# Performance work log

Measured on AMD Instinct MI355X. Metric: run time of the kernel, lower is better.

## Reference

```python
import jax, jax.numpy as jnp
import numpy as np

N = 100000   # nodes
E = 3200000  # edges (avg degree 32)
G = 1024     # graphs in batch
H = 16       # hidden_dim


def setup_inputs() -> dict:
    key = jax.random.key(0)
    ks = jax.random.split(key, 12)
    p = lambda k, s: jax.random.normal(k, s, dtype=jnp.float32) * 0.1
    return {
        "types": jax.random.randint(ks[0], (N,), 0, 3),
        "pos": jax.random.randint(ks[1], (N,), 0, 3),
        "edge_index": jax.random.randint(ks[2], (2, E), 0, N),
        "batch": jnp.sort(jax.random.randint(ks[3], (N,), 0, G)),
        "W1": p(ks[4], (3, H)), "b1": jnp.zeros((H,), jnp.float32),
        "W2": p(ks[5], (3, H)), "b2": jnp.zeros((H,), jnp.float32),
        "Wg0": p(ks[6], (2 * H, H)), "bg0": jnp.zeros((H,), jnp.float32),
        "Wg1": p(ks[7], (H, H)), "bg1": jnp.zeros((H,), jnp.float32),
        "Wg2": p(ks[8], (H, H)), "bg2": jnp.zeros((H,), jnp.float32),
        "Wo": p(ks[9], (H, 1)), "bo": jnp.zeros((1,), jnp.float32),
    }


def reference(types, pos, edge_index, batch, W1, b1, W2, b2,
              Wg0, bg0, Wg1, bg1, Wg2, bg2, Wo, bo):
    # one-hot encode + linear embed
    xt = jax.nn.one_hot(types, 3, dtype=jnp.float32) @ W1 + b1   # [N, H]
    xp = jax.nn.one_hot(pos, 3, dtype=jnp.float32) @ W2 + b2     # [N, H]
    z = jnp.concatenate([xt, xp], axis=-1)                        # [N, 2H]

    src, dst = edge_index[0], edge_index[1]
    # GCN symmetric normalization with self-loops (gcn_norm)
    deg = jax.ops.segment_sum(jnp.ones((E,), jnp.float32), dst, num_segments=N) + 1.0
    dis = jax.lax.rsqrt(deg)                                      # D^{-1/2}
    edge_coef = (dis[src] * dis[dst])[:, None]                    # [E, 1]
    self_coef = (dis * dis)[:, None]                              # [N, 1]

    def gcn_conv(x, W, b):
        h = x @ W                                                 # [N, H]
        agg = jax.ops.segment_sum(h[src] * edge_coef, dst, num_segments=N)
        return agg + h * self_coef + b

    z = jax.nn.relu(gcn_conv(z, Wg0, bg0))  # dropout=0.2 is train-only; eval mode
    z = jax.nn.relu(gcn_conv(z, Wg1, bg1))
    z = gcn_conv(z, Wg2, bg2)               # no act after last layer

    # global_mean_pool over graph ids
    cnt = jax.ops.segment_sum(jnp.ones((N,), jnp.float32), batch, num_segments=G)
    pooled = jax.ops.segment_sum(z, batch, num_segments=G) / jnp.maximum(cnt, 1.0)[:, None]
    return pooled @ Wo + bo                                       # [G, 1]
```

## Files before the change

### kernel.cpp

```cpp
#include <hip/hip_runtime.h>
#include <hip/hip_fp16.h>

#define NN 100000
#define NE 3200000
#define NG 1024
#define NP 100352
#define NBUCK 391
#define NBLK 256
#define CHUNK ((NE + NBLK - 1) / NBLK)
#define WINCAP 12288

static __device__ inline void acc_u2(float4& acc, uint2 u) {
    __half2* ph = reinterpret_cast<__half2*>(&u);
    float2 lo = __half22float2(ph[0]);
    float2 hi = __half22float2(ph[1]);
    acc.x += lo.x; acc.y += lo.y; acc.z += hi.x; acc.w += hi.y;
}
static __device__ inline uint2 pack4(float a, float b, float c, float d) {
    __half2 lo = __floats2half2_rn(a, b);
    __half2 hi = __floats2half2_rn(c, d);
    uint2 u;
    u.x = *reinterpret_cast<unsigned int*>(&lo);
    u.y = *reinterpret_cast<unsigned int*>(&hi);
    return u;
}
static __device__ inline float4 shfl_xor4(float4 v, int m) {
    float4 r;
    r.x = __shfl_xor(v.x, m); r.y = __shfl_xor(v.y, m);
    r.z = __shfl_xor(v.z, m); r.w = __shfl_xor(v.w, m);
    return r;
}

__global__ void hist_buckets(const int* __restrict__ dst, int* __restrict__ bcnt) {
    __shared__ int sm[NBUCK];
    int tid = threadIdx.x;
    for (int i = tid; i < NBUCK; i += 256) sm[i] = 0;
    __syncthreads();
    int s = blockIdx.x * CHUNK, e = min(NE, s + CHUNK);
    for (int i = s + tid; i < e; i += 256) atomicAdd(&sm[dst[i] >> 8], 1);
    __syncthreads();
    for (int i = tid; i < NBUCK; i += 256)
        if (sm[i]) atomicAdd(&bcnt[i], sm[i]);
}

__global__ void scan_buckets(const int* __restrict__ bcnt, int* __restrict__ bbase) {
    __shared__ int tmp[512];
    int tid = threadIdx.x;
    int v = (tid < NBUCK) ? bcnt[tid] : 0;
    tmp[tid] = v;
    __syncthreads();
    for (int off = 1; off < 512; off <<= 1) {
        int t = (tid >= off) ? tmp[tid - off] : 0;
        __syncthreads();
        tmp[tid] += t;
        __syncthreads();
    }
    if (tid < NBUCK) bbase[tid] = tmp[tid] - v;
}

__global__ void partition(const int* __restrict__ src, const int* __restrict__ dst,
                          const int* __restrict__ bbase, int* __restrict__ bfill,
                          int* __restrict__ part) {
    __shared__ int smh[NBUCK];
    __shared__ int smc[NBUCK];
    int tid = threadIdx.x;
    for (int i = tid; i < NBUCK; i += 256) smh[i] = 0;
    __syncthreads();
    int s = blockIdx.x * CHUNK, e = min(NE, s + CHUNK);
    for (int i = s + tid; i < e; i += 256) atomicAdd(&smh[dst[i] >> 8], 1);
    __syncthreads();
    for (int i = tid; i < NBUCK; i += 256) {
        int c = smh[i];
        smc[i] = c ? (bbase[i] + atomicAdd(&bfill[i], c)) : 0;
    }
    __syncthreads();
    for (int i = s + tid; i < e; i += 256) {
        int d = dst[i];
        int b = d >> 8;
        int p = atomicAdd(&smc[b], 1);
        part[p] = src[i] | ((d & 255) << 17);
    }
}

__global__ void build_csr(const int* __restrict__ part, const int* __restrict__ bbase,
                          const int* __restrict__ bcnt, const int* __restrict__ types,
                          const int* __restrict__ pos, int* __restrict__ cnt,
                          int* __restrict__ offs, float* __restrict__ dis,
                          unsigned int* __restrict__ pk, int* __restrict__ srcs) {
    __shared__ int sm_cnt[256];
    __shared__ int sm_off[256];
    __shared__ int sm_cur[256];
    __shared__ int sm_win[WINCAP];
    int b = blockIdx.x, tid = threadIdx.x;
    int base = bbase[b], m = bcnt[b];
    sm_cnt[tid] = 0;
    __syncthreads();
    for (int i = tid; i < m; i += 256) atomicAdd(&sm_cnt[part[base + i] >> 17], 1);
    __syncthreads();
    int v = sm_cnt[tid];
    sm_off[tid] = v;
    __syncthreads();
    for (int off = 1; off < 256; off <<= 1) {
        int t = (tid >= off) ? sm_off[tid - off] : 0;
        __syncthreads();
        sm_off[tid] += t;
        __syncthreads();
    }
    int excl = sm_off[tid] - v;
    int n = b * 256 + tid;
    if (n < NN) {
        cnt[n] = v;
        offs[n] = base + excl;
        float dv = rsqrtf((float)v + 1.0f);
        dis[n] = dv;
        int cls = types[n] * 3 + pos[n];
        __half hd = __float2half_rn(dv);
        pk[n] = ((unsigned int)cls << 16) | (unsigned int)__half_as_ushort(hd);
    }
    sm_cur[tid] = excl;
    __syncthreads();
    if (m <= WINCAP) {
        for (int i = tid; i < m; i += 256) {
            int p = part[base + i];
            int l = atomicAdd(&sm_cur[p >> 17], 1);
            sm_win[l] = p & 0x1FFFF;
        }
        __syncthreads();
        for (int i = tid; i < m; i += 256) srcs[base + i] = sm_win[i];
    } else {
        for (int i = tid; i < m; i += 256) {
            int p = part[base + i];
            int l = atomicAdd(&sm_cur[p >> 17], 1);
            srcs[base + l] = p & 0x1FFFF;
        }
    }
}

__global__ void agg0_tf(const unsigned int* __restrict__ pk,
                        const int* __restrict__ srcs, const int* __restrict__ offs,
                        const int* __restrict__ cnt, const float* __restrict__ dis,
                        const float* __restrict__ W1, const float* __restrict__ b1,
                        const float* __restrict__ W2, const float* __restrict__ b2,
                        const float* __restrict__ Wg0, const float* __restrict__ bg0,
                        const float* __restrict__ Wg1, uint2* __restrict__ hs_out) {
    __shared__ float sV[144];
    __shared__ float sW[256];
    int tid = threadIdx.x;
    sW[tid] = Wg1[tid];
    if (tid < 144) {
        int c = tid >> 4, f = tid & 15;
        int ty = c / 3, pp = c % 3;
        float a = 0.f;
#pragma unroll
        for (int k = 0; k < 16; k++) a += (W1[ty * 16 + k] + b1[k]) * Wg0[k * 16 + f];
#pragma unroll
        for (int k = 0; k < 16; k++) a += (W2[pp * 16 + k] + b2[k]) * Wg0[(16 + k) * 16 + f];
        sV[tid] = a;
    }
    __syncthreads();
    int gid = blockIdx.x * 256 + tid;
    int n = gid >> 1, h = gid & 1;
    if (n >= NN) return;
    int beg = offs[n], deg = cnt[n];
    int half = deg >> 1;
    int lo = beg + (h ? half : 0);
    int hi = beg + (h ? deg : half);

    float a0 = 0.f, a1 = 0.f, a2 = 0.f, a3 = 0.f, a4 = 0.f;
    float a5 = 0.f, a6 = 0.f, a7 = 0.f, a8 = 0.f;
#define ACCP(P)                                                       \
    do {                                                              \
        unsigned int _p = (P);                                        \
        int _c = (int)(_p >> 16);                                     \
        float _d = __half2float(__ushort_as_half((unsigned short)(_p & 0xFFFFu))); \
        a0 += (_c == 0) ? _d : 0.f;  a1 += (_c == 1) ? _d : 0.f;      \
        a2 += (_c == 2) ? _d : 0.f;  a3 += (_c == 3) ? _d : 0.f;      \
        a4 += (_c == 4) ? _d : 0.f;  a5 += (_c == 5) ? _d : 0.f;      \
        a6 += (_c == 6) ? _d : 0.f;  a7 += (_c == 7) ? _d : 0.f;      \
        a8 += (_c == 8) ? _d : 0.f;                                   \
    } while (0)
    int i = lo;
    for (; i + 4 <= hi; i += 4) {
        int s0 = srcs[i + 0];
        int s1 = srcs[i + 1];
        int s2 = srcs[i + 2];
        int s3 = srcs[i + 3];
        unsigned int p0 = pk[s0];
        unsigned int p1 = pk[s1];
        unsigned int p2 = pk[s2];
        unsigned int p3 = pk[s3];
        ACCP(p0); ACCP(p1); ACCP(p2); ACCP(p3);
    }
    for (; i < hi; i++) ACCP(pk[srcs[i]]);

    a0 += __shfl_xor(a0, 1); a1 += __shfl_xor(a1, 1); a2 += __shfl_xor(a2, 1);
    a3 += __shfl_xor(a3, 1); a4 += __shfl_xor(a4, 1); a5 += __shfl_xor(a5, 1);
    a6 += __shfl_xor(a6, 1); a7 += __shfl_xor(a7, 1); a8 += __shfl_xor(a8, 1);
    ACCP(pk[n]);
#undef ACCP

    float dn = dis[n];
    float acc[9] = {a0, a1, a2, a3, a4, a5, a6, a7, a8};
    float pre[16];
#pragma unroll
    for (int f = 0; f < 16; f++) {
        float a = 0.f;
#pragma unroll
        for (int c = 0; c < 9; c++) a += acc[c] * sV[c * 16 + f];
        a = fmaf(a, dn, bg0[f]);
        pre[f] = fmaxf(a, 0.f);
    }
    if (h == 0) {
        float hv[16];
#pragma unroll
        for (int f2 = 0; f2 < 16; f2++) hv[f2] = 0.f;
#pragma unroll
        for (int f = 0; f < 16; f++) {
            float z = pre[f];
#pragma unroll
            for (int f2 = 0; f2 < 16; f2++) hv[f2] += z * sW[f * 16 + f2];
        }
        uint2* op = hs_out + (size_t)n * 4;
#pragma unroll
        for (int q = 0; q < 4; q++)
            op[q] = pack4(hv[q * 4] * dn, hv[q * 4 + 1] * dn,
                          hv[q * 4 + 2] * dn, hv[q * 4 + 3] * dn);
    }
}

template <int RELU, int FUSE_POOL>
__global__ void agg_tf(const uint2* __restrict__ hs, const int* __restrict__ srcs,
                       const int* __restrict__ offs, const int* __restrict__ cnt,
                       const float* __restrict__ dis, const float* __restrict__ bias,
                       const float* __restrict__ Wn, uint2* __restrict__ hs_out,
                       const int* __restrict__ batch,
                       float* __restrict__ pool, int* __restrict__ gcnt) {
    __shared__ float sW[256];
    int tid = threadIdx.x;
    if (!FUSE_POOL) {
        sW[tid] = Wn[tid];
        __syncthreads();
    }
    int gid = blockIdx.x * 256 + tid;
    int n = gid >> 2, q = gid & 3;
    if (n >= NN) return;
    int beg = offs[n], deg = cnt[n];
    float dn = dis[n];
    float4 acc = make_float4(0.f, 0.f, 0.f, 0.f);
    int i = 0;
    for (; i + 4 <= deg; i += 4) {
        int s0 = srcs[beg + i + 0];
        int s1 = srcs[beg + i + 1];
        int s2 = srcs[beg + i + 2];
        int s3 = srcs[beg + i + 3];
        uint2 a0 = hs[(size_t)s0 * 4 + q];
        uint2 a1 = hs[(size_t)s1 * 4 + q];
        uint2 a2 = hs[(size_t)s2 * 4 + q];
        uint2 a3 = hs[(size_t)s3 * 4 + q];
        acc_u2(acc, a0); acc_u2(acc, a1); acc_u2(acc, a2); acc_u2(acc, a3);
    }
    for (; i < deg; i++) {
        int s = srcs[beg + i];
        acc_u2(acc, hs[(size_t)s * 4 + q]);
    }
    acc_u2(acc, hs[(size_t)n * 4 + q]);
    float4 b4 = ((const float4*)bias)[q];
    acc.x = fmaf(acc.x, dn, b4.x);
    acc.y = fmaf(acc.y, dn, b4.y);
    acc.z = fmaf(acc.z, dn, b4.z);
    acc.w = fmaf(acc.w, dn, b4.w);
    if (RELU) {
        acc.x = fmaxf(acc.x, 0.f); acc.y = fmaxf(acc.y, 0.f);
        acc.z = fmaxf(acc.z, 0.f); acc.w = fmaxf(acc.w, 0.f);
    }
    if (FUSE_POOL) {
        float4 w4 = ((const float4*)Wn)[q];
        float s = acc.x * w4.x + acc.y * w4.y + acc.z * w4.z + acc.w * w4.w;
        s += __shfl_xor(s, 1);
        s += __shfl_xor(s, 2);
        if (q == 0) {
            int g = batch[n];
            atomicAdd(&pool[g], s);
            atomicAdd(&gcnt[g], 1);
        }
    } else {
        float4 vals[4];
        vals[0] = acc;
        vals[1] = shfl_xor4(acc, 1);
        vals[2] = shfl_xor4(acc, 2);
        vals[3] = shfl_xor4(acc, 3);
        const float4* sW4 = (const float4*)sW;
        float4 hv = make_float4(0.f, 0.f, 0.f, 0.f);
#pragma unroll
        for (int m = 0; m < 4; m++) {
            float4 v = vals[m];
            int rb = (q ^ m) << 2;
            float4 w;
            w = sW4[(rb + 0) * 4 + q];
            hv.x += v.x * w.x; hv.y += v.x * w.y; hv.z += v.x * w.z; hv.w += v.x * w.w;
            w = sW4[(rb + 1) * 4 + q];
            hv.x += v.y * w.x; hv.y += v.y * w.y; hv.z += v.y * w.z; hv.w += v.y * w.w;
            w = sW4[(rb + 2) * 4 + q];
            hv.x += v.z * w.x; hv.y += v.z * w.y; hv.z += v.z * w.z; hv.w += v.z * w.w;
            w = sW4[(rb + 3) * 4 + q];
            hv.x += v.w * w.x; hv.y += v.w * w.y; hv.z += v.w * w.z; hv.w += v.w * w.w;
        }
        hs_out[(size_t)n * 4 + q] = pack4(hv.x * dn, hv.y * dn, hv.z * dn, hv.w * dn);
    }
}

__global__ void finalize(const float* __restrict__ pool, const int* __restrict__ gcnt,
                         const float* __restrict__ bo, float* __restrict__ out) {
    int g = blockIdx.x * 256 + threadIdx.x;
    if (g < NG) {
        float c = fmaxf((float)gcnt[g], 1.0f);
        out[g] = pool[g] / c + bo[0];
    }
}

extern "C" void kernel_launch(void* const* d_in, const int* in_sizes, int n_in,
                              void* d_out, int out_size, void* d_ws, size_t ws_size,
                              hipStream_t stream) {
    const int*   types = (const int*)d_in[0];
    const int*   pos   = (const int*)d_in[1];
    const int*   ei    = (const int*)d_in[2];
    const int*   batch = (const int*)d_in[3];
    const float* W1  = (const float*)d_in[4];
    const float* b1  = (const float*)d_in[5];
    const float* W2  = (const float*)d_in[6];
    const float* b2  = (const float*)d_in[7];
    const float* Wg0 = (const float*)d_in[8];
    const float* bg0 = (const float*)d_in[9];
    const float* Wg1 = (const float*)d_in[10];
    const float* bg1 = (const float*)d_in[11];
    const float* Wg2 = (const float*)d_in[12];
    const float* bg2 = (const float*)d_in[13];
    const float* Wo  = (const float*)d_in[14];
    const float* bo  = (const float*)d_in[15];
    float* out = (float*)d_out;

    const int* esrc = ei;
    const int* edst = ei + NE;

    int*   bcnt  = (int*)d_ws;
    int*   bfill = bcnt + 512;
    float* pool  = (float*)(bfill + 512);
    int*   gcnt  = (int*)(pool + NG);
    int*   bbase = gcnt + NG;
    int*   cnt   = bbase + 512;
    int*   offs  = cnt + NP;
    float* dis   = (float*)(offs + NP);
    unsigned int* pk = (unsigned int*)(dis + NP);
    int*   srcs  = (int*)(pk + NP);
    int*   part  = srcs + NE;
    uint2* hsA   = (uint2*)part;
    uint2* hsB   = (uint2*)(part + NE / 2);
    (void)ws_size; (void)n_in; (void)in_sizes; (void)out_size;

    hipMemsetAsync(d_ws, 0, (size_t)(1024 + 2 * NG) * sizeof(int), stream);

    const int QB  = (NN * 4 + 255) / 256;
    const int QB2 = (NN * 2 + 255) / 256;

    hist_buckets<<<NBLK, 256, 0, stream>>>(edst, bcnt);
    scan_buckets<<<1, 512, 0, stream>>>(bcnt, bbase);
    partition<<<NBLK, 256, 0, stream>>>(esrc, edst, bbase, bfill, part);
    build_csr<<<NBUCK, 256, 0, stream>>>(part, bbase, bcnt, types, pos,
                                         cnt, offs, dis, pk, srcs);

    agg0_tf<<<QB2, 256, 0, stream>>>(pk, srcs, offs, cnt, dis, W1, b1, W2, b2,
                                     Wg0, bg0, Wg1, hsA);
    agg_tf<1, 0><<<QB, 256, 0, stream>>>(hsA, srcs, offs, cnt, dis, bg1, Wg2, hsB,
                                         batch, pool, gcnt);
    agg_tf<0, 1><<<QB, 256, 0, stream>>>(hsB, srcs, offs, cnt, dis, bg2, Wo, hsA ,
                                         batch, pool, gcnt);

    finalize<<<(NG + 255) / 256, 256, 0, stream>>>(pool, gcnt, bo, out);
}
```

Measured before the change: 325.7 us.

## Stream feature table through LDS in slices for sorted-neighbor aggregation

build_csr now sorts each node's neighbor list by source slice (4096-row chunks) using per-node, per-slice counters. The two later GCN aggregation kernels are rewritten so that each 512-thread block streams the whole half-precision feature table through shared memory slice by slice. Each thread handles one node and consumes its sorted neighbors from LDS, instead of doing random global gathers with four threads per node. The aim is to turn random gathers into coalesced streaming reads. The cost is that every one of the 256 blocks reads the full feature table, adds many barriers, and runs a serial per-thread loop over neighbors.

Result: slower. 391.3 us (+20.1%).

```diff
diff --git a/kernel.cpp b/kernel.cpp
--- a/kernel.cpp
+++ b/kernel.cpp
@@ -9,12 +9,15 @@
 #define NBLK 256
 #define CHUNK ((NE + NBLK - 1) / NBLK)
 #define WINCAP 12288
-
-static __device__ inline void acc_u2(float4& acc, uint2 u) {
+#define NSL 25
+#define SLROWS 4096
+#define NPB 392
+
+static __device__ inline void addu2(float* a, uint2 u) {
     __half2* ph = reinterpret_cast<__half2*>(&u);
-    float2 lo = __half22float2(ph[0]);
-    float2 hi = __half22float2(ph[1]);
-    acc.x += lo.x; acc.y += lo.y; acc.z += hi.x; acc.w += hi.y;
+    float2 f0 = __half22float2(ph[0]);
+    float2 f1 = __half22float2(ph[1]);
+    a[0] += f0.x; a[1] += f0.y; a[2] += f1.x; a[3] += f1.y;
 }
 static __device__ inline uint2 pack4(float a, float b, float c, float d) {
     __half2 lo = __floats2half2_rn(a, b);
@@ -24,12 +27,6 @@
     u.y = *reinterpret_cast<unsigned int*>(&hi);
     return u;
 }
-static __device__ inline float4 shfl_xor4(float4 v, int m) {
-    float4 r;
-    r.x = __shfl_xor(v.x, m); r.y = __shfl_xor(v.y, m);
-    r.z = __shfl_xor(v.z, m); r.w = __shfl_xor(v.w, m);
-    return r;
-}
 
 __global__ void hist_buckets(const int* __restrict__ dst, int* __restrict__ bcnt) {
     __shared__ int sm[NBUCK];
@@ -87,26 +84,36 @@
                           const int* __restrict__ pos, int* __restrict__ cnt,
                           int* __restrict__ offs, float* __restrict__ dis,
                           unsigned int* __restrict__ pk, int* __restrict__ srcs) {
-    __shared__ int sm_cnt[256];
-    __shared__ int sm_off[256];
-    __shared__ int sm_cur[256];
-    __shared__ int sm_win[WINCAP];
+    __shared__ int cnt2[256 * NSL];
+    __shared__ int cur2[256 * NSL];
+    __shared__ int tmp[256];
+    __shared__ int win[WINCAP];
     int b = blockIdx.x, tid = threadIdx.x;
     int base = bbase[b], m = bcnt[b];
-    sm_cnt[tid] = 0;
-    __syncthreads();
-    for (int i = tid; i < m; i += 256) atomicAdd(&sm_cnt[part[base + i] >> 17], 1);
-    __syncthreads();
-    int v = sm_cnt[tid];
-    sm_off[tid] = v;
+    for (int i = tid; i < 256 * NSL; i += 256) cnt2[i] = 0;
+    __syncthreads();
+    for (int i = tid; i < m; i += 256) {
+        int p = part[base + i];
+        int key = (p >> 17) * NSL + ((p & 0x1FFFF) >> 12);
+        atomicAdd(&cnt2[key], 1);
+    }
+    __syncthreads();
+    int run = 0;
+    for (int j = 0; j < NSL; j++) {
+        int c = cnt2[tid * NSL + j];
+        cur2[tid * NSL + j] = run;
+        run += c;
+    }
+    int v = run;
+    tmp[tid] = v;
     __syncthreads();
     for (int off = 1; off < 256; off <<= 1) {
-        int t = (tid >= off) ? sm_off[tid - off] : 0;
-        __syncthreads();
-        sm_off[tid] += t;
-        __syncthreads();
-    }
-    int excl = sm_off[tid] - v;
+        int t = (tid >= off) ? tmp[tid - off] : 0;
+        __syncthreads();
+        tmp[tid] += t;
+        __syncthreads();
+    }
+    int excl = tmp[tid] - v;
     int n = b * 256 + tid;
     if (n < NN) {
         cnt[n] = v;
@@ -114,23 +121,25 @@
         float dv = rsqrtf((float)v + 1.0f);
         dis[n] = dv;
         int cls = types[n] * 3 + pos[n];
-        __half hd = __float2half_rn(dv);
-        pk[n] = ((unsigned int)cls << 16) | (unsigned int)__half_as_ushort(hd);
-    }
-    sm_cur[tid] = excl;
+        pk[n] = ((unsigned int)cls << 16) |
+                (unsigned int)__half_as_ushort(__float2half_rn(dv));
+    }
+    for (int j = 0; j < NSL; j++) cur2[tid * NSL + j] += excl;
     __syncthreads();
     if (m <= WINCAP) {
         for (int i = tid; i < m; i += 256) {
             int p = part[base + i];
-            int l = atomicAdd(&sm_cur[p >> 17], 1);
-            sm_win[l] = p & 0x1FFFF;
-        }
-        __syncthreads();
-        for (int i = tid; i < m; i += 256) srcs[base + i] = sm_win[i];
+            int key = (p >> 17) * NSL + ((p & 0x1FFFF) >> 12);
+            int l = atomicAdd(&cur2[key], 1);
+            win[l] = p & 0x1FFFF;
+        }
+        __syncthreads();
+        for (int i = tid; i < m; i += 256) srcs[base + i] = win[i];
     } else {
         for (int i = tid; i < m; i += 256) {
             int p = part[base + i];
-            int l = atomicAdd(&sm_cur[p >> 17], 1);
+            int key = (p >> 17) * NSL + ((p & 0x1FFFF) >> 12);
+            int l = atomicAdd(&cur2[key], 1);
             srcs[base + l] = p & 0x1FFFF;
         }
     }
@@ -229,83 +238,100 @@
 }
 
 template <int RELU, int FUSE_POOL>
-__global__ void agg_tf(const uint2* __restrict__ hs, const int* __restrict__ srcs,
-                       const int* __restrict__ offs, const int* __restrict__ cnt,
-                       const float* __restrict__ dis, const float* __restrict__ bias,
-                       const float* __restrict__ Wn, uint2* __restrict__ hs_out,
-                       const int* __restrict__ batch,
-                       float* __restrict__ pool, int* __restrict__ gcnt) {
-    __shared__ float sW[256];
-    int tid = threadIdx.x;
-    if (!FUSE_POOL) {
-        sW[tid] = Wn[tid];
-        __syncthreads();
-    }
-    int gid = blockIdx.x * 256 + tid;
-    int n = gid >> 2, q = gid & 3;
-    if (n >= NN) return;
-    int beg = offs[n], deg = cnt[n];
-    float dn = dis[n];
-    float4 acc = make_float4(0.f, 0.f, 0.f, 0.f);
-    int i = 0;
-    for (; i + 4 <= deg; i += 4) {
-        int s0 = srcs[beg + i + 0];
-        int s1 = srcs[beg + i + 1];
-        int s2 = srcs[beg + i + 2];
-        int s3 = srcs[beg + i + 3];
-        uint2 a0 = hs[(size_t)s0 * 4 + q];
-        uint2 a1 = hs[(size_t)s1 * 4 + q];
-        uint2 a2 = hs[(size_t)s2 * 4 + q];
-        uint2 a3 = hs[(size_t)s3 * 4 + q];
-        acc_u2(acc, a0); acc_u2(acc, a1); acc_u2(acc, a2); acc_u2(acc, a3);
-    }
-    for (; i < deg; i++) {
-        int s = srcs[beg + i];
-        acc_u2(acc, hs[(size_t)s * 4 + q]);
-    }
-    acc_u2(acc, hs[(size_t)n * 4 + q]);
-    float4 b4 = ((const float4*)bias)[q];
-    acc.x = fmaf(acc.x, dn, b4.x);
-    acc.y = fmaf(acc.y, dn, b4.y);
-    acc.z = fmaf(acc.z, dn, b4.z);
-    acc.w = fmaf(acc.w, dn, b4.w);
-    if (RELU) {
-        acc.x = fmaxf(acc.x, 0.f); acc.y = fmaxf(acc.y, 0.f);
-        acc.z = fmaxf(acc.z, 0.f); acc.w = fmaxf(acc.w, 0.f);
+__global__ __launch_bounds__(512) void agg_lds(
+        const uint2* __restrict__ hs, const int* __restrict__ srcs,
+        const int* __restrict__ offs, const int* __restrict__ cnt,
+        const float* __restrict__ dis, const float* __restrict__ bias,
+        const float* __restrict__ Wn, uint2* __restrict__ hs_out,
+        const int* __restrict__ batch, float* __restrict__ pool,
+        int* __restrict__ gcnt) {
+    __shared__ uint2 sl[4 * SLROWS];
+    int tid = threadIdx.x, b = blockIdx.x;
+    int n = b * NPB + tid;
+    bool act = (tid < NPB) && (n < NN);
+    int beg = 0, deg = 0;
+    float dn = 0.f;
+    if (act) { beg = offs[n]; deg = cnt[n]; dn = dis[n]; }
+    float acc[16];
+#pragma unroll
+    for (int j = 0; j < 16; j++) acc[j] = 0.f;
+    int cur = 0;
+    int sv = (act && deg > 0) ? srcs[beg] : 0x7FFFFFFF;
+    const uint4* hs4 = (const uint4*)hs;
+
+    for (int s = 0; s < NSL; s++) {
+        __syncthreads();
+#pragma unroll
+        for (int k = 0; k < 8; k++) {
+            int r = tid + k * 512;
+            uint4 A = hs4[(size_t)(s * SLROWS + r) * 2];
+            uint4 B = hs4[(size_t)(s * SLROWS + r) * 2 + 1];
+            sl[r]              = make_uint2(A.x, A.y);
+            sl[SLROWS + r]     = make_uint2(A.z, A.w);
+            sl[2 * SLROWS + r] = make_uint2(B.x, B.y);
+            sl[3 * SLROWS + r] = make_uint2(B.z, B.w);
+        }
+        __syncthreads();
+        int hi = (s + 1) * SLROWS;
+        while (sv < hi) {
+            int rl = sv - s * SLROWS;
+            uint2 p0 = sl[rl];
+            uint2 p1 = sl[SLROWS + rl];
+            uint2 p2 = sl[2 * SLROWS + rl];
+            uint2 p3 = sl[3 * SLROWS + rl];
+            addu2(acc + 0, p0);  addu2(acc + 4, p1);
+            addu2(acc + 8, p2);  addu2(acc + 12, p3);
+            cur++;
+            sv = (cur < deg) ? srcs[beg + cur] : 0x7FFFFFFF;
+        }
+    }
+
+    float z[16];
+    if (act) {
+        const uint4* hp = (const uint4*)(hs + (size_t)n * 4);
+        uint4 ha = hp[0], hb = hp[1];
+        addu2(acc + 0, make_uint2(ha.x, ha.y));
+        addu2(acc + 4, make_uint2(ha.z, ha.w));
+        addu2(acc + 8, make_uint2(hb.x, hb.y));
+        addu2(acc + 12, make_uint2(hb.z, hb.w));
+#pragma unroll
+        for (int j = 0; j < 16; j++) {
+            float a = fmaf(acc[j], dn, bias[j]);
+            z[j] = RELU ? fmaxf(a, 0.f) : a;
+        }
     }
     if (FUSE_POOL) {
-        float4 w4 = ((const float4*)Wn)[q];
-        float s = acc.x * w4.x + acc.y * w4.y + acc.z * w4.z + acc.w * w4.w;
-        s += __shfl_xor(s, 1);
-        s += __shfl_xor(s, 2);
-        if (q == 0) {
+        if (act) {
+            float ssum = 0.f;
+#pragma unroll
+            for (int j = 0; j < 16; j++) ssum += z[j] * Wn[j];
             int g = batch[n];
-            atomicAdd(&pool[g], s);
+            atomicAdd(&pool[g], ssum);
             atomicAdd(&gcnt[g], 1);
         }
     } else {
-        float4 vals[4];
-        vals[0] = acc;
-        vals[1] = shfl_xor4(acc, 1);
-        vals[2] = shfl_xor4(acc, 2);
-        vals[3] = shfl_xor4(acc, 3);
-        const float4* sW4 = (const float4*)sW;
-        float4 hv = make_float4(0.f, 0.f, 0.f, 0.f);
-#pragma unroll
-        for (int m = 0; m < 4; m++) {
-            float4 v = vals[m];
-            int rb = (q ^ m) << 2;
-            float4 w;
-            w = sW4[(rb + 0) * 4 + q];
-            hv.x += v.x * w.x; hv.y += v.x * w.y; hv.z += v.x * w.z; hv.w += v.x * w.w;
-            w = sW4[(rb + 1) * 4 + q];
-            hv.x += v.y * w.x; hv.y += v.y * w.y; hv.z += v.y * w.z; hv.w += v.y * w.w;
-            w = sW4[(rb + 2) * 4 + q];
-            hv.x += v.z * w.x; hv.y += v.z * w.y; hv.z += v.z * w.z; hv.w += v.z * w.w;
-            w = sW4[(rb + 3) * 4 + q];
-            hv.x += v.w * w.x; hv.y += v.w * w.y; hv.z += v.w * w.z; hv.w += v.w * w.w;
-        }
-        hs_out[(size_t)n * 4 + q] = pack4(hv.x * dn, hv.y * dn, hv.z * dn, hv.w * dn);
+        __syncthreads();
+        float* sW = (float*)sl;
+        if (tid < 256) sW[tid] = Wn[tid];
+        __syncthreads();
+        if (act) {
+            float hv[16];
+#pragma unroll
+            for (int f2 = 0; f2 < 16; f2++) hv[f2] = 0.f;
+#pragma unroll
+            for (int f = 0; f < 16; f++) {
+                float zf = z[f];
+#pragma unroll
+                for (int f2 = 0; f2 < 16; f2++) hv[f2] += zf * sW[f * 16 + f2];
+            }
+            uint2 t0 = pack4(hv[0] * dn, hv[1] * dn, hv[2] * dn, hv[3] * dn);
+            uint2 t1 = pack4(hv[4] * dn, hv[5] * dn, hv[6] * dn, hv[7] * dn);
+            uint2 t2 = pack4(hv[8] * dn, hv[9] * dn, hv[10] * dn, hv[11] * dn);
+            uint2 t3 = pack4(hv[12] * dn, hv[13] * dn, hv[14] * dn, hv[15] * dn);
+            uint4* op = (uint4*)(hs_out + (size_t)n * 4);
+            op[0] = make_uint4(t0.x, t0.y, t1.x, t1.y);
+            op[1] = make_uint4(t2.x, t2.y, t3.x, t3.y);
+        }
     }
 }
 
@@ -359,7 +385,6 @@
 
     hipMemsetAsync(d_ws, 0, (size_t)(1024 + 2 * NG) * sizeof(int), stream);
 
-    const int QB  = (NN * 4 + 255) / 256;
     const int QB2 = (NN * 2 + 255) / 256;
 
     hist_buckets<<<NBLK, 256, 0, stream>>>(edst, bcnt);
@@ -370,10 +395,10 @@
 
     agg0_tf<<<QB2, 256, 0, stream>>>(pk, srcs, offs, cnt, dis, W1, b1, W2, b2,
                                      Wg0, bg0, Wg1, hsA);
-    agg_tf<1, 0><<<QB, 256, 0, stream>>>(hsA, srcs, offs, cnt, dis, bg1, Wg2, hsB,
-                                         batch, pool, gcnt);
-    agg_tf<0, 1><<<QB, 256, 0, stream>>>(hsB, srcs, offs, cnt, dis, bg2, Wo, hsA ,
-                                         batch, pool, gcnt);
+    agg_lds<1, 0><<<256, 512, 0, stream>>>(hsA, srcs, offs, cnt, dis, bg1, Wg2,
+                                           hsB, batch, pool, gcnt);
+    agg_lds<0, 1><<<256, 512, 0, stream>>>(hsB, srcs, offs, cnt, dis, bg2, Wo,
+                                           hsA , batch, pool, gcnt);
 
     finalize<<<(NG + 255) / 256, 256, 0, stream>>>(pool, gcnt, bo, out);
 }
```
